# Kernel optimization log

Hardware: AMD Instinct MI355X
Metric: run time of the kernel (lower is better)

Reference implementation:

```python
import jax, jax.numpy as jnp
import numpy as np
from jax import lax

B, S, F = 64, 63, 64          # batch, window length, num_past_features
T, NF, OUT = 12, 63, 1        # pred_sequence_length, forecast feats, output_size
C, K = 32, 3                  # hidden channels, kernel size
DILS = (1, 2, 4, 8, 16)       # S = (K-1)*sum(DILS)+1 = 63 -> conv stack reduces to length 1


def setup_inputs() -> dict:
    key = jax.random.key(0)
    ks = jax.random.split(key, 8)
    sc = 0.1
    x = jax.random.normal(ks[0], (B, S, F), dtype=jnp.float32)
    x_forecasts = jax.random.normal(ks[1], (B, T, NF), dtype=jnp.float32)
    # per-feature conv stacks stored as grouped-conv weights (feature_group_count=F)
    w0 = jax.random.normal(ks[2], (F * C, 1, K), dtype=jnp.float32) * sc
    b0 = jnp.zeros((F * C,), dtype=jnp.float32)
    wmid = jax.random.normal(ks[3], (3, F * C, C, K), dtype=jnp.float32) * sc
    bmid = jnp.zeros((3, F * C), dtype=jnp.float32)
    wlast = jax.random.normal(ks[4], (F * 1, C, K), dtype=jnp.float32) * sc
    blast = jnp.zeros((F,), dtype=jnp.float32)
    linW = jax.random.normal(ks[5], (OUT, F + NF), dtype=jnp.float32) * sc
    linb = jnp.zeros((OUT,), dtype=jnp.float32)
    return dict(x=x, x_forecasts=x_forecasts, w0=w0, b0=b0, wmid=wmid,
                bmid=bmid, wlast=wlast, blast=blast, linW=linW, linb=linb)


def _dconv(h, w, d):
    # h: [B, F*Cin, L]; grouped dilated conv, one group per past feature
    return lax.conv_general_dilated(h, w, window_strides=(1,), padding='VALID',
                                    rhs_dilation=(d,),
                                    dimension_numbers=('NCH', 'OIH', 'NCH'),
                                    feature_group_count=F)


def _step(xw, xf, w0, b0, wmid, bmid, wlast, blast, linW, linb):
    # xw: [B, S, F] window; xf: [B, NF] forecast features for this step
    h = jnp.transpose(xw, (0, 2, 1))                       # [B, F, S]
    h = jax.nn.relu(_dconv(h, w0, DILS[0]) + b0[None, :, None])
    for k in range(3):
        h = jax.nn.relu(_dconv(h, wmid[k], DILS[k + 1]) + bmid[k][None, :, None])
    h = _dconv(h, wlast, DILS[4]) + blast[None, :, None]   # [B, F, 1], no final relu
    feat = jnp.concatenate([h[:, :, 0], xf], axis=1)       # [B, F+NF]
    return feat @ linW.T + linb                            # [B, OUT]


def reference(x, x_forecasts, w0, b0, wmid, bmid, wlast, blast, linW, linb):
    params = (w0, b0, wmid, bmid, wlast, blast, linW, linb)
    out0 = _step(x, x_forecasts[:, 0], *params)

    def body(carry, xs):
        xw, prev = carry
        xf_i, xf_ip1 = xs
        add = jnp.concatenate([xf_i, prev], axis=1)[:, None, :]   # [B,1,F] since NF+OUT=F
        xw = jnp.concatenate([xw[:, 1:, :], add], axis=1)          # slide window
        out = _step(xw, xf_ip1, *params)
        return (xw, out), out

    xs = (jnp.swapaxes(x_forecasts[:, :-1], 0, 1),   # [T-1, B, NF]
          jnp.swapaxes(x_forecasts[:, 1:], 0, 1))
    _, outs = lax.scan(body, (x, out0), xs)          # [T-1, B, OUT]
    return jnp.swapaxes(jnp.concatenate([out0[None], outs], axis=0), 0, 1)  # [B, T, OUT]
```

## Files before the change

### kernel.cpp

```cpp
#include <hip/hip_runtime.h>


typedef _Float16 f16;
typedef _Float16 h2 __attribute__((ext_vector_type(2)));
typedef _Float16 f16x4 __attribute__((ext_vector_type(4)));
typedef _Float16 f16x8 __attribute__((ext_vector_type(8)));
typedef float f32x16 __attribute__((ext_vector_type(16)));

#define OFF_H4    0
#define OFF_ST    49152
#define ST_L0     0
#define ST_L1     128
#define ST_L2     384
#define ST_L3     896
#define ST_STRIDE 1760
#define OFF_H40   161792
#define OFF_WPK   161856
#define OFF_RECH  456768
#define OFF_PRM   461376
#define OFF_XFT   462400

#define WPK_N   589824
#define RECH_END (WPK_N + 9216)
#define PRM_END  (RECH_END + 1024)
#define TOT_N    (PRM_END + 49152)

#define RPAD 36
#define NROW 100

__global__ __launch_bounds__(256) void repack_w(
    const float* __restrict__ wmid, const float* __restrict__ w0,
    const float* __restrict__ b0, const float* __restrict__ bmid,
    const float* __restrict__ wlast, const float* __restrict__ blast,
    const float* __restrict__ linW, const float* __restrict__ linb,
    const float* __restrict__ xfc, f16* __restrict__ wpk,
    float* __restrict__ ws)
{
  const int idx = blockIdx.x * 256 + threadIdx.x;
  if (idx < WPK_N) {
    const int j = idx & 7, r1 = idx >> 3;
    const int lane = r1 & 63, r2 = r1 >> 6;
    const int h = r2 & 1, r3 = r2 >> 1;
    const int t = r3 % 3, r4 = r3 / 3;
    const int f = r4 & 63, m = r4 >> 6;
    const int co = lane & 31;
    const int ci = h * 16 + (lane >> 5) * 8 + j;
    wpk[idx] = (f16)wmid[m * 196608 + (f * 32 + co) * 96 + ci * 3 + t];
  } else if (idx < RECH_END) {
    const int r = idx - WPK_N;
    const int e = r & 7, lane = (r >> 3) & 63, q = r >> 9;
    const int i = q * 8 + e;
    const int m = i / 48, r2 = i % 48;
    const int k = r2 >> 4, ci = r2 & 15;
    const int c = lane & 31, cib = (lane >> 5) * 16;
    ((f16*)(ws + OFF_RECH))[r] =
        (f16)wmid[m * 196608 + (2016 + c) * 96 + (cib + ci) * 3 + k];
  } else if (idx < PRM_END) {
    const int r = idx - RECH_END;
    const int e = r & 3, lane = (r >> 2) & 63, q = r >> 8;
    const int i = q * 4 + e;
    const int c = lane & 31;
    float v = 0.f;
    if (i < 3)        v = w0[(2016 + c) * 3 + i];
    else if (i == 3)  v = b0[2016 + c];
    else if (i < 7)   v = bmid[(i - 4) * 2048 + 2016 + c];
    else if (i < 10)  v = wlast[63 * 96 + c * 3 + (i - 7)];
    else if (i == 10) v = blast[63];
    else if (i == 11) v = linW[63];
    else if (i == 12) v = linb[0];
    ws[OFF_PRM + r] = v;
  } else if (idx < TOT_N) {
    const int r = idx - PRM_END;
    const int b = r / 768, rem = r % 768;
    const int q = rem >> 8, lane = (rem >> 2) & 63, e = rem & 3;
    const int i = q * 4 + e;
    ws[OFF_XFT + r] = (lane < 63 && i < 12) ? xfc[(b * 12 + i) * 63 + lane] : 0.f;
  }
}

__device__ __forceinline__ void mfma_tile(
    int m, const f16* IN, f16* OUT, int d, int base,
    const f16* __restrict__ wpk, int f, int lane, const float* sBias)
{
  const int lg = lane >> 5;
  const int col = base + (lane & 31);

  f16x8 afr[6];
  const f16* wb = wpk + (m * 64 + f) * 6 * 512 + lane * 8;
#pragma unroll
  for (int u = 0; u < 6; ++u)
    afr[u] = *(const f16x8*)(wb + u * 512);

  f32x16 acc;
#pragma unroll
  for (int r = 0; r < 16; ++r)
    acc[r] = sBias[(r & 3) + 8 * (r >> 2) + 4 * lg];

#pragma unroll
  for (int t = 0; t < 3; ++t) {
#pragma unroll
    for (int h = 0; h < 2; ++h) {
      const f16* bp = IN + (col + t * d) * RPAD + h * 16 + lg * 8;
      f16x4 lo = *(const f16x4*)bp;
      f16x4 hi = *(const f16x4*)(bp + 4);
      f16x8 b = __builtin_shufflevector(lo, hi, 0, 1, 2, 3, 4, 5, 6, 7);
      acc = __builtin_amdgcn_mfma_f32_32x32x16_f16(afr[t * 2 + h], b, acc, 0, 0, 0);
    }
  }

#pragma unroll
  for (int q = 0; q < 4; ++q) {
    const int co0 = q * 8 + 4 * lg;
    f16x4 w;
#pragma unroll
    for (int e = 0; e < 4; ++e)
      w[e] = (f16)fmaxf(acc[q * 4 + e], 0.f);
    *(f16x4*)(OUT + col * RPAD + co0) = w;
  }
}

__global__ __launch_bounds__(256) void tcn_pre(
    const float* __restrict__ x, const float* __restrict__ xfc,
    const float* __restrict__ w0, const float* __restrict__ b0,
    const float* __restrict__ bmid,
    const float* __restrict__ wlast, const float* __restrict__ blast,
    const f16* __restrict__ wpk, float* __restrict__ ws)
{
  const int blk = blockIdx.x;
  const int b = blk >> 6;
  const int f = blk & 63;
  const bool lastf = (f == 63);
  const int tid = threadIdx.x;
  const int lane = tid & 63;
  const int g = __builtin_amdgcn_readfirstlane(tid >> 6);

  __shared__ float sIn[80];
  __shared__ float sBias[3][32];
  __shared__ f16 actA[NROW * RPAD];
  __shared__ f16 actB[NROW * RPAD];

  for (int t = tid; t < 80; t += 256) {
    float v = 0.f;
    if (t < 63)                 v = x[(b * 63 + t) * 64 + f];
    else if (t < 74 && !lastf)  v = xfc[(b * 12 + (t - 63)) * 63 + f];
    sIn[t] = v;
  }
  if (tid < 96) sBias[tid >> 5][tid & 31] = bmid[(tid >> 5) * 2048 + f * 32 + (tid & 31)];
  for (int i = tid; i < (NROW - 72) * RPAD; i += 256) actA[72 * RPAD + i] = (f16)0.f;
  for (int i = tid; i < (NROW - 68) * RPAD; i += 256) actB[68 * RPAD + i] = (f16)0.f;
  __syncthreads();

  {
    const float* wb  = w0 + (f * 32 + g * 8) * 3;
    const float* bbp = b0 + f * 32 + g * 8;
#pragma unroll
    for (int it = 0; it < 2; ++it) {
      const int p = lane + it * 64;
      if (p < 72) {
        const float i0 = sIn[p], i1 = sIn[p + 1], i2 = sIn[p + 2];
        f16x4 wv[2];
#pragma unroll
        for (int j = 0; j < 8; ++j) {
          float v = fmaf(wb[j * 3 + 0], i0,
                    fmaf(wb[j * 3 + 1], i1,
                    fmaf(wb[j * 3 + 2], i2, bbp[j])));
          wv[j >> 2][j & 3] = (f16)fmaxf(v, 0.f);
        }
        *(f16x4*)(actA + p * RPAD + g * 8)     = wv[0];
        *(f16x4*)(actA + p * RPAD + g * 8 + 4) = wv[1];
      }
    }
  }
  __syncthreads();

  float* st = ws + OFF_ST + b * ST_STRIDE;

  if (lastf) {
    for (int t = tid; t < 128; t += 256)
      st[ST_L0 + t] = (float)actA[(57 + (t >> 5)) * RPAD + (t & 31)];
  }
  if (g < 3) mfma_tile(0, actA, actB, 2, g * 32, wpk, f, lane, sBias[0]);
  __syncthreads();

  if (lastf) {
    for (int t = tid; t < 256; t += 256)
      st[ST_L1 + t] = (float)actB[(49 + (t >> 5)) * RPAD + (t & 31)];
  }
  if (g < 2) mfma_tile(1, actB, actA, 4, g * 32, wpk, f, lane, sBias[1]);
  __syncthreads();

  if (lastf) {
    for (int t = tid; t < 512; t += 256)
      st[ST_L2 + t] = (float)actA[(33 + (t >> 5)) * RPAD + (t & 31)];
  }
  if (g < 2) mfma_tile(2, actA, actB, 8, g * 32, wpk, f, lane, sBias[2]);
  __syncthreads();

  if (lastf) {
    for (int t = tid; t < 864; t += 256)
      st[ST_L3 + t] = (float)actB[(1 + (t >> 5)) * RPAD + (t & 31)];
  }
  if (tid < 12) {
    const int p = tid;
    float acc = blast[f];
    const float* wl = wlast + f * 96;
#pragma unroll
    for (int k = 0; k < 3; ++k) {
      const int row = p + 16 * k;
#pragma unroll
      for (int ci0 = 0; ci0 < 32; ci0 += 4) {
        f16x4 av = *(const f16x4*)(actB + row * RPAD + ci0);
#pragma unroll
        for (int e = 0; e < 4; ++e)
          acc = fmaf(wl[(ci0 + e) * 3 + k], (float)av[e], acc);
      }
    }
    if (!lastf) {
      ws[OFF_H4 + b * 768 + (p >> 2) * 256 + f * 4 + (p & 3)] = acc;
    } else {
      ws[OFF_H4 + b * 768 + (p >> 2) * 256 + 63 * 4 + (p & 3)] = 0.f;
      if (p == 0) ws[OFF_H40 + b] = acc;
    }
  }
}


__device__ __forceinline__ float fd2(h2 a, h2 b, float c) {
#if __has_builtin(__builtin_amdgcn_fdot2)
  return __builtin_amdgcn_fdot2(a, b, c, false);
#else
  return fmaf((float)a[0], (float)b[0], fmaf((float)a[1], (float)b[1], c));
#endif
}

__device__ __forceinline__ float dotv(f16x8 w, f16x8 a, float acc) {
  h2 w0 = {w[0], w[1]}, a0 = {a[0], a[1]};
  h2 w1 = {w[2], w[3]}, a1 = {a[2], a[3]};
  h2 w2 = {w[4], w[5]}, a2 = {a[4], a[5]};
  h2 w3 = {w[6], w[7]}, a3 = {a[6], a[7]};
  acc = fd2(w0, a0, acc);
  acc = fd2(w1, a1, acc);
  acc = fd2(w2, a2, acc);
  acc = fd2(w3, a3, acc);
  return acc;
}

__device__ __forceinline__ f16x8 combineh(f16x8 lo, f16x8 hi) {
  f16x8 s = lo + hi;
#pragma unroll
  for (int i = 0; i < 8; ++i) s[i] = (s[i] > (f16)0.f) ? s[i] : (f16)0.f;
  return s;
}

__device__ __forceinline__ void load16f(const float* p, float* r) {
  const float4* q = reinterpret_cast<const float4*>(p);
  const float4 v0 = q[0], v1 = q[1], v2 = q[2], v3 = q[3];
  r[0]=v0.x;  r[1]=v0.y;  r[2]=v0.z;  r[3]=v0.w;
  r[4]=v1.x;  r[5]=v1.y;  r[6]=v1.z;  r[7]=v1.w;
  r[8]=v2.x;  r[9]=v2.y;  r[10]=v2.z; r[11]=v2.w;
  r[12]=v3.x; r[13]=v3.y; r[14]=v3.z; r[15]=v3.w;
}

__global__ __launch_bounds__(64, 1) void tcn_seq(
    const float* __restrict__ x,
    const float* __restrict__ linW,
    const float* __restrict__ ws, float* __restrict__ out)
{
  const int b = blockIdx.x;
  const int tid = threadIdx.x;
  const int c = tid & 31;
  const int h = tid >> 5;
  const int cib = h * 16;

  __shared__ __align__(16) f16 L0h[15 * 32];
  __shared__ __align__(16) f16 L1p[2][19 * 32];
  __shared__ __align__(16) f16 L2p[2][27 * 32];
  __shared__ __align__(16) f16 wseqh[18 * 64 * 8];
  __shared__ __align__(16) float qs[32];
  __shared__ float preArr[12];

  const float* stp = ws + OFF_ST + b * ST_STRIDE;

  for (int t = tid; t < 128; t += 64) L0h[t] = (f16)stp[ST_L0 + t];
  for (int t = tid; t < 256; t += 64) { L1p[0][t] = (f16)stp[ST_L1 + t]; L1p[1][t] = (f16)0.f; }
  for (int t = tid; t < 512; t += 64) { L2p[0][t] = (f16)stp[ST_L2 + t]; L2p[1][t] = (f16)0.f; }

  {
    const f16* rech = (const f16*)(ws + OFF_RECH);
#pragma unroll
    for (int q = 0; q < 18; ++q)
      *(f16x8*)(wseqh + (q * 64 + tid) * 8) = *(const f16x8*)(rech + (q * 64 + tid) * 8);
  }

  float prm[16];
  {
    const float* tab = ws + OFF_PRM;
#pragma unroll
    for (int q = 0; q < 4; ++q) {
      const float4 v = *reinterpret_cast<const float4*>(tab + (q * 64 + tid) * 4);
      prm[q * 4 + 0] = v.x; prm[q * 4 + 1] = v.y;
      prm[q * 4 + 2] = v.z; prm[q * 4 + 3] = v.w;
    }
  }
  const float w00 = prm[0],  w01 = prm[1],  w02 = prm[2],  b00 = prm[3];
  const float bm0 = prm[4],  bm1 = prm[5],  bm2 = prm[6];
  const float wl0c = prm[7], wl1c = prm[8], wl2c = prm[9];
  const float bl = prm[10],  lw63 = prm[11], lb0 = prm[12];

  const float xv61 = x[(b * 63 + 61) * 64 + 63];
  const float xv62 = x[(b * 63 + 62) * 64 + 63];
  const float h40v = ws[OFF_H40 + b];

  float accv[12];
  {
    float lw = 0.f, lwx = 0.f;
    if (tid < 63) { lw = linW[tid]; lwx = linW[64 + tid]; }
    float h4v[12], xv[12];
#pragma unroll
    for (int q = 0; q < 3; ++q) {
      const float4 hv  = *reinterpret_cast<const float4*>(ws + OFF_H4 + b * 768 + q * 256 + tid * 4);
      const float4 xvv = *reinterpret_cast<const float4*>(ws + OFF_XFT + b * 768 + q * 256 + tid * 4);
      h4v[q*4+0] = hv.x; h4v[q*4+1] = hv.y; h4v[q*4+2] = hv.z; h4v[q*4+3] = hv.w;
      xv[q*4+0] = xvv.x; xv[q*4+1] = xvv.y; xv[q*4+2] = xvv.z; xv[q*4+3] = xvv.w;
    }
#pragma unroll
    for (int i = 0; i < 12; ++i) accv[i] = fmaf(lw, h4v[i], lwx * xv[i]);

    if (tid < 32) {
#pragma unroll
      for (int i = 1; i < 12; ++i) {
        const float qc = fmaf(wl0c, stp[ST_L3 + (i - 1) * 32 + tid],
                              wl1c * stp[ST_L3 + (i + 15) * 32 + tid]);
        accv[i] = fmaf(lw63, qc, accv[i]);
      }
    }
#pragma unroll
    for (int r = 1; r < 64; r <<= 1) {
#pragma unroll
      for (int i = 0; i < 12; ++i) accv[i] += __shfl_xor(accv[i], r);
    }
  }
  if (tid == 0) {
#pragma unroll
    for (int i = 1; i < 12; ++i) preArr[i] = accv[i] + lb0 + lw63 * bl;
  }
  __syncthreads();

  const f16* wbase = wseqh;
  asm volatile("" : "+v"(wbase));

  const float out0 = fmaf(lw63, h40v, accv[0] + lb0);
  if (tid == 0) out[b * 12 + 0] = out0;
  float o1 = out0, o2 = xv62, o3 = xv61;

#pragma unroll 1
  for (int s = 1; s < 12; ++s) {
    const float preS = preArr[s];

    const float nL0 = fmaxf(fmaf(w00, o3, fmaf(w01, o2, fmaf(w02, o1, b00))), 0.f);
    L0h[(3 + s) * 32 + c] = (f16)nL0;

    float v1;
    {
      const f16* wp = wbase + (0 * 6 * 64 + tid) * 8;
      f16x8 W0 = *(const f16x8*)(wp);
      f16x8 W1 = *(const f16x8*)(wp + 64 * 8);
      f16x8 W2 = *(const f16x8*)(wp + 2 * 64 * 8);
      f16x8 W3 = *(const f16x8*)(wp + 3 * 64 * 8);
      f16x8 W4 = *(const f16x8*)(wp + 4 * 64 * 8);
      f16x8 W5 = *(const f16x8*)(wp + 5 * 64 * 8);
      const f16* r0p = L0h + (s - 1) * 32 + cib;
      const f16* r1p = L0h + (s + 1) * 32 + cib;
      const f16* np  = L0h + (3 + s) * 32 + cib;
      f16x8 R0a = *(const f16x8*)r0p, R0b = *(const f16x8*)(r0p + 8);
      f16x8 R1a = *(const f16x8*)r1p, R1b = *(const f16x8*)(r1p + 8);
      f16x8 Na  = *(const f16x8*)np,  Nb  = *(const f16x8*)(np + 8);
      float a0 = dotv(W0, R0a, 0.f), a1 = dotv(W1, R0b, 0.f);
      a0 = dotv(W2, R1a, a0);        a1 = dotv(W3, R1b, a1);
      a0 = dotv(W4, Na, a0);         a1 = dotv(W5, Nb, a1);
      v1 = a0 + a1 + (h == 0 ? bm0 : 0.f);
    }
    L1p[h][(7 + s) * 32 + c] = (f16)v1;

    float v2;
    {
      const f16* wp = wbase + (1 * 6 * 64 + tid) * 8;
      f16x8 W0 = *(const f16x8*)(wp);
      f16x8 W1 = *(const f16x8*)(wp + 64 * 8);
      f16x8 W2 = *(const f16x8*)(wp + 2 * 64 * 8);
      f16x8 W3 = *(const f16x8*)(wp + 3 * 64 * 8);
      f16x8 W4 = *(const f16x8*)(wp + 4 * 64 * 8);
      f16x8 W5 = *(const f16x8*)(wp + 5 * 64 * 8);
      const int i0 = (s - 1) * 32 + cib, i1 = (s + 3) * 32 + cib, in = (7 + s) * 32 + cib;
      f16x8 R0a = combineh(*(const f16x8*)(&L1p[0][i0]),     *(const f16x8*)(&L1p[1][i0]));
      f16x8 R0b = combineh(*(const f16x8*)(&L1p[0][i0 + 8]), *(const f16x8*)(&L1p[1][i0 + 8]));
      f16x8 R1a = combineh(*(const f16x8*)(&L1p[0][i1]),     *(const f16x8*)(&L1p[1][i1]));
      f16x8 R1b = combineh(*(const f16x8*)(&L1p[0][i1 + 8]), *(const f16x8*)(&L1p[1][i1 + 8]));
      f16x8 Na  = combineh(*(const f16x8*)(&L1p[0][in]),     *(const f16x8*)(&L1p[1][in]));
      f16x8 Nb  = combineh(*(const f16x8*)(&L1p[0][in + 8]), *(const f16x8*)(&L1p[1][in + 8]));
      float a0 = dotv(W0, R0a, 0.f), a1 = dotv(W1, R0b, 0.f);
      a0 = dotv(W2, R1a, a0);        a1 = dotv(W3, R1b, a1);
      a0 = dotv(W4, Na, a0);         a1 = dotv(W5, Nb, a1);
      v2 = a0 + a1 + (h == 0 ? bm1 : 0.f);
    }
    L2p[h][(15 + s) * 32 + c] = (f16)v2;

    float v3;
    {
      const f16* wp = wbase + (2 * 6 * 64 + tid) * 8;
      f16x8 W0 = *(const f16x8*)(wp);
      f16x8 W1 = *(const f16x8*)(wp + 64 * 8);
      f16x8 W2 = *(const f16x8*)(wp + 2 * 64 * 8);
      f16x8 W3 = *(const f16x8*)(wp + 3 * 64 * 8);
      f16x8 W4 = *(const f16x8*)(wp + 4 * 64 * 8);
      f16x8 W5 = *(const f16x8*)(wp + 5 * 64 * 8);
      const int i0 = (s - 1) * 32 + cib, i1 = (s + 7) * 32 + cib, in = (15 + s) * 32 + cib;
      f16x8 R0a = combineh(*(const f16x8*)(&L2p[0][i0]),     *(const f16x8*)(&L2p[1][i0]));
      f16x8 R0b = combineh(*(const f16x8*)(&L2p[0][i0 + 8]), *(const f16x8*)(&L2p[1][i0 + 8]));
      f16x8 R1a = combineh(*(const f16x8*)(&L2p[0][i1]),     *(const f16x8*)(&L2p[1][i1]));
      f16x8 R1b = combineh(*(const f16x8*)(&L2p[0][i1 + 8]), *(const f16x8*)(&L2p[1][i1 + 8]));
      f16x8 Na  = combineh(*(const f16x8*)(&L2p[0][in]),     *(const f16x8*)(&L2p[1][in]));
      f16x8 Nb  = combineh(*(const f16x8*)(&L2p[0][in + 8]), *(const f16x8*)(&L2p[1][in + 8]));
      float a0 = dotv(W0, R0a, 0.f), a1 = dotv(W1, R0b, 0.f);
      a0 = dotv(W2, R1a, a0);        a1 = dotv(W3, R1b, a1);
      a0 = dotv(W4, Na, a0);         a1 = dotv(W5, Nb, a1);
      v3 = a0 + a1 + (h == 0 ? bm2 : 0.f);
    }
    v3 += __shfl_xor(v3, 32);
    const float nL3 = fmaxf(v3, 0.f);

    if (h == 0) qs[c] = wl2c * nL3;
    float qa[16], qb[16];
    load16f(qs, qa); load16f(qs + 16, qb);
    float s0 = 0.f, s1 = 0.f, s2 = 0.f, s3 = 0.f;
#pragma unroll
    for (int i = 0; i < 16; i += 4) {
      s0 += qa[i + 0] + qb[i + 0];
      s1 += qa[i + 1] + qb[i + 1];
      s2 += qa[i + 2] + qb[i + 2];
      s3 += qa[i + 3] + qb[i + 3];
    }
    const float S = (s0 + s1) + (s2 + s3);
    const float outs = fmaf(lw63, S, preS);
    if (tid == 0) out[b * 12 + s] = outs;
    o3 = o2; o2 = o1; o1 = outs;
  }
}


extern "C" void kernel_launch(void* const* d_in, const int* in_sizes, int n_in,
                              void* d_out, int out_size, void* d_ws, size_t ws_size,
                              hipStream_t stream) {
  const float* x     = (const float*)d_in[0];
  const float* xfc   = (const float*)d_in[1];
  const float* w0    = (const float*)d_in[2];
  const float* b0    = (const float*)d_in[3];
  const float* wmid  = (const float*)d_in[4];
  const float* bmid  = (const float*)d_in[5];
  const float* wlast = (const float*)d_in[6];
  const float* blast = (const float*)d_in[7];
  const float* linW  = (const float*)d_in[8];
  const float* linb  = (const float*)d_in[9];
  float* out = (float*)d_out;
  float* ws  = (float*)d_ws;
  f16* wpk = (f16*)(ws + OFF_WPK);

  repack_w<<<(TOT_N + 255) / 256, 256, 0, stream>>>(
      wmid, w0, b0, bmid, wlast, blast, linW, linb, xfc, wpk, ws);
  tcn_pre<<<64 * 64, 256, 0, stream>>>(x, xfc, w0, b0, bmid, wlast, blast, wpk, ws);
  tcn_seq<<<64, 64, 0, stream>>>(x, linW, ws, out);
}
```

Measured before the change: 42.66 us.

## Fuse weight repack into tcn_pre by staging fp32 weights through LDS per block

Removes the separate repack_w launch that converted all mid-layer weights to a packed fp16 layout in global memory. Each tcn_pre block now loads its feature's fp32 weight slice directly, converts it to fp16 into shared memory, and builds MFMA A-fragments from LDS. The small remaining repack work (last-feature params, forecast transpose) runs in extra blocks appended to the tcn_pre grid. This trades a kernel launch and a global write/read pass for redundant per-block weight loads (each weight read by 64 batch blocks) and extra barriers.

```diff
diff --git a/kernel.cpp b/kernel.cpp
--- a/kernel.cpp
+++ b/kernel.cpp
@@ -15,81 +15,52 @@
 #define ST_L3     896
 #define ST_STRIDE 1760
 #define OFF_H40   161792
-#define OFF_WPK   161856
-#define OFF_RECH  456768
-#define OFF_PRM   461376
-#define OFF_XFT   462400
-
-#define WPK_N   589824
-#define RECH_END (WPK_N + 9216)
-#define PRM_END  (RECH_END + 1024)
-#define TOT_N    (PRM_END + 49152)
+#define OFF_RECH  161856
+#define OFF_PRM   166464
+#define OFF_XFT   167488
+
+#define RECH_N 9216
+#define TAIL_N 59392
 
 #define RPAD 36
 #define NROW 100
 
-__global__ __launch_bounds__(256) void repack_w(
-    const float* __restrict__ wmid, const float* __restrict__ w0,
-    const float* __restrict__ b0, const float* __restrict__ bmid,
-    const float* __restrict__ wlast, const float* __restrict__ blast,
-    const float* __restrict__ linW, const float* __restrict__ linb,
-    const float* __restrict__ xfc, f16* __restrict__ wpk,
-    float* __restrict__ ws)
+__device__ __forceinline__ void stage_wrow(
+    const float* __restrict__ wmid, int m, int f, int tid, f16* wrow)
 {
-  const int idx = blockIdx.x * 256 + threadIdx.x;
-  if (idx < WPK_N) {
-    const int j = idx & 7, r1 = idx >> 3;
-    const int lane = r1 & 63, r2 = r1 >> 6;
-    const int h = r2 & 1, r3 = r2 >> 1;
-    const int t = r3 % 3, r4 = r3 / 3;
-    const int f = r4 & 63, m = r4 >> 6;
-    const int co = lane & 31;
-    const int ci = h * 16 + (lane >> 5) * 8 + j;
-    wpk[idx] = (f16)wmid[m * 196608 + (f * 32 + co) * 96 + ci * 3 + t];
-  } else if (idx < RECH_END) {
-    const int r = idx - WPK_N;
-    const int e = r & 7, lane = (r >> 3) & 63, q = r >> 9;
-    const int i = q * 8 + e;
-    const int m = i / 48, r2 = i % 48;
-    const int k = r2 >> 4, ci = r2 & 15;
-    const int c = lane & 31, cib = (lane >> 5) * 16;
-    ((f16*)(ws + OFF_RECH))[r] =
-        (f16)wmid[m * 196608 + (2016 + c) * 96 + (cib + ci) * 3 + k];
-  } else if (idx < PRM_END) {
-    const int r = idx - RECH_END;
-    const int e = r & 3, lane = (r >> 2) & 63, q = r >> 8;
-    const int i = q * 4 + e;
-    const int c = lane & 31;
-    float v = 0.f;
-    if (i < 3)        v = w0[(2016 + c) * 3 + i];
-    else if (i == 3)  v = b0[2016 + c];
-    else if (i < 7)   v = bmid[(i - 4) * 2048 + 2016 + c];
-    else if (i < 10)  v = wlast[63 * 96 + c * 3 + (i - 7)];
-    else if (i == 10) v = blast[63];
-    else if (i == 11) v = linW[63];
-    else if (i == 12) v = linb[0];
-    ws[OFF_PRM + r] = v;
-  } else if (idx < TOT_N) {
-    const int r = idx - PRM_END;
-    const int b = r / 768, rem = r % 768;
-    const int q = rem >> 8, lane = (rem >> 2) & 63, e = rem & 3;
-    const int i = q * 4 + e;
-    ws[OFF_XFT + r] = (lane < 63 && i < 12) ? xfc[(b * 12 + i) * 63 + lane] : 0.f;
-  }
-}
-
-__device__ __forceinline__ void mfma_tile(
-    int m, const f16* IN, f16* OUT, int d, int base,
-    const f16* __restrict__ wpk, int f, int lane, const float* sBias)
+  const float* src = wmid + m * 196608 + f * 3072 + tid * 12;
+  f16* dst = wrow + (tid >> 3) * 100 + (tid & 7) * 12;
+#pragma unroll
+  for (int u = 0; u < 3; ++u) {
+    const float4 v = *reinterpret_cast<const float4*>(src + u * 4);
+    dst[u * 4 + 0] = (f16)v.x; dst[u * 4 + 1] = (f16)v.y;
+    dst[u * 4 + 2] = (f16)v.z; dst[u * 4 + 3] = (f16)v.w;
+  }
+}
+
+__device__ __forceinline__ void mfma_tile2(
+    const f16* IN, f16* OUT, int d, int base,
+    const f16* __restrict__ wrow, int lane, const float* sBias)
 {
   const int lg = lane >> 5;
-  const int col = base + (lane & 31);
+  const int co = lane & 31;
+  const int col = base + co;
 
   f16x8 afr[6];
-  const f16* wb = wpk + (m * 64 + f) * 6 * 512 + lane * 8;
-#pragma unroll
-  for (int u = 0; u < 6; ++u)
-    afr[u] = *(const f16x8*)(wb + u * 512);
+#pragma unroll
+  for (int h = 0; h < 2; ++h) {
+    const f16* wp = wrow + co * 100 + (h * 16 + lg * 8) * 3;
+    f16x4 w4[6];
+#pragma unroll
+    for (int u = 0; u < 6; ++u) w4[u] = *(const f16x4*)(wp + u * 4);
+#pragma unroll
+    for (int t = 0; t < 3; ++t)
+#pragma unroll
+      for (int j = 0; j < 8; ++j) {
+        const int o = 3 * j + t;
+        afr[t * 2 + h][j] = w4[o >> 2][o & 3];
+      }
+  }
 
   f32x16 acc;
 #pragma unroll
@@ -122,15 +93,51 @@
 __global__ __launch_bounds__(256) void tcn_pre(
     const float* __restrict__ x, const float* __restrict__ xfc,
     const float* __restrict__ w0, const float* __restrict__ b0,
-    const float* __restrict__ bmid,
+    const float* __restrict__ wmid, const float* __restrict__ bmid,
     const float* __restrict__ wlast, const float* __restrict__ blast,
-    const f16* __restrict__ wpk, float* __restrict__ ws)
+    const float* __restrict__ linW, const float* __restrict__ linb,
+    float* __restrict__ ws)
 {
   const int blk = blockIdx.x;
+  const int tid = threadIdx.x;
+
+  if (blk >= 4096) {
+    const int idx = (blk - 4096) * 256 + tid;
+    if (idx < RECH_N) {
+      const int e = idx & 7, lane = (idx >> 3) & 63, q = idx >> 9;
+      const int i = q * 8 + e;
+      const int m = i / 48, r2 = i % 48;
+      const int k = r2 >> 4, ci = r2 & 15;
+      const int c = lane & 31, cib = (lane >> 5) * 16;
+      ((f16*)(ws + OFF_RECH))[idx] =
+          (f16)wmid[m * 196608 + (2016 + c) * 96 + (cib + ci) * 3 + k];
+    } else if (idx < RECH_N + 1024) {
+      const int r = idx - RECH_N;
+      const int e = r & 3, lane = (r >> 2) & 63, q = r >> 8;
+      const int i = q * 4 + e;
+      const int c = lane & 31;
+      float v = 0.f;
+      if (i < 3)        v = w0[(2016 + c) * 3 + i];
+      else if (i == 3)  v = b0[2016 + c];
+      else if (i < 7)   v = bmid[(i - 4) * 2048 + 2016 + c];
+      else if (i < 10)  v = wlast[63 * 96 + c * 3 + (i - 7)];
+      else if (i == 10) v = blast[63];
+      else if (i == 11) v = linW[63];
+      else if (i == 12) v = linb[0];
+      ws[OFF_PRM + r] = v;
+    } else if (idx < TAIL_N) {
+      const int r = idx - (RECH_N + 1024);
+      const int b = r / 768, rem = r % 768;
+      const int q = rem >> 8, lane = (rem >> 2) & 63, e = rem & 3;
+      const int i = q * 4 + e;
+      ws[OFF_XFT + r] = (lane < 63 && i < 12) ? xfc[(b * 12 + i) * 63 + lane] : 0.f;
+    }
+    return;
+  }
+
   const int b = blk >> 6;
   const int f = blk & 63;
   const bool lastf = (f == 63);
-  const int tid = threadIdx.x;
   const int lane = tid & 63;
   const int g = __builtin_amdgcn_readfirstlane(tid >> 6);
 
@@ -138,6 +145,7 @@
   __shared__ float sBias[3][32];
   __shared__ f16 actA[NROW * RPAD];
   __shared__ f16 actB[NROW * RPAD];
+  __shared__ __align__(8) f16 wrow[32 * 100];
 
   for (int t = tid; t < 80; t += 256) {
     float v = 0.f;
@@ -148,6 +156,7 @@
   if (tid < 96) sBias[tid >> 5][tid & 31] = bmid[(tid >> 5) * 2048 + f * 32 + (tid & 31)];
   for (int i = tid; i < (NROW - 72) * RPAD; i += 256) actA[72 * RPAD + i] = (f16)0.f;
   for (int i = tid; i < (NROW - 68) * RPAD; i += 256) actB[68 * RPAD + i] = (f16)0.f;
+  stage_wrow(wmid, 0, f, tid, wrow);
   __syncthreads();
 
   {
@@ -179,21 +188,27 @@
     for (int t = tid; t < 128; t += 256)
       st[ST_L0 + t] = (float)actA[(57 + (t >> 5)) * RPAD + (t & 31)];
   }
-  if (g < 3) mfma_tile(0, actA, actB, 2, g * 32, wpk, f, lane, sBias[0]);
-  __syncthreads();
-
+  if (g < 3) mfma_tile2(actA, actB, 2, g * 32, wrow, lane, sBias[0]);
+  __syncthreads();
+
+  stage_wrow(wmid, 1, f, tid, wrow);
   if (lastf) {
     for (int t = tid; t < 256; t += 256)
       st[ST_L1 + t] = (float)actB[(49 + (t >> 5)) * RPAD + (t & 31)];
   }
-  if (g < 2) mfma_tile(1, actB, actA, 4, g * 32, wpk, f, lane, sBias[1]);
-  __syncthreads();
-
+  __syncthreads();
+
+  if (g < 2) mfma_tile2(actB, actA, 4, g * 32, wrow, lane, sBias[1]);
+  __syncthreads();
+
+  stage_wrow(wmid, 2, f, tid, wrow);
   if (lastf) {
     for (int t = tid; t < 512; t += 256)
       st[ST_L2 + t] = (float)actA[(33 + (t >> 5)) * RPAD + (t & 31)];
   }
-  if (g < 2) mfma_tile(2, actA, actB, 8, g * 32, wpk, f, lane, sBias[2]);
+  __syncthreads();
+
+  if (g < 2) mfma_tile2(actA, actB, 8, g * 32, wrow, lane, sBias[2]);
   __syncthreads();
 
   if (lastf) {
@@ -463,10 +478,8 @@
   const float* linb  = (const float*)d_in[9];
   float* out = (float*)d_out;
   float* ws  = (float*)d_ws;
-  f16* wpk = (f16*)(ws + OFF_WPK);
-
-  repack_w<<<(TOT_N + 255) / 256, 256, 0, stream>>>(
-      wmid, w0, b0, bmid, wlast, blast, linW, linb, xfc, wpk, ws);
-  tcn_pre<<<64 * 64, 256, 0, stream>>>(x, xfc, w0, b0, bmid, wlast, blast, wpk, ws);
+
+  tcn_pre<<<4096 + 232, 256, 0, stream>>>(
+      x, xfc, w0, b0, wmid, bmid, wlast, blast, linW, linb, ws);
   tcn_seq<<<64, 64, 0, stream>>>(x, linW, ws, out);
 }
```

Measured after the change: 41.85 us. About the same (-1.9%).
